# Kernel tuning notes

Hardware: AMD Instinct MI355X
Metric: run time of the kernel (lower is better)

## Reference

```python
import jax, jax.numpy as jnp
import numpy as np

B, N, E = 8, 10000, 160000
F_IN, HID, EMB = 5, 128, 256
A_LAST, S_STEP = 10, 1


def _gcn_layer(x, src, dst, W, b, num_nodes):
    # PyG GCNConv: h = x @ W^T, add self-loops, symmetric norm, scatter-add, + bias
    h = x @ W.T
    loops = jnp.arange(num_nodes, dtype=src.dtype)
    src2 = jnp.concatenate([src, loops])
    dst2 = jnp.concatenate([dst, loops])
    deg = jax.ops.segment_sum(jnp.ones_like(dst2, dtype=h.dtype), dst2, num_segments=num_nodes)
    dinv = jnp.where(deg > 0, jax.lax.rsqrt(deg), 0.0)
    norm = dinv[src2] * dinv[dst2]                     # [E+N]
    msgs = h[src2] * norm[:, None]                     # gather + scale
    out = jax.ops.segment_sum(msgs, dst2, num_segments=num_nodes)
    return out + b


def setup_inputs() -> dict:
    key = jax.random.key(0)
    ks = jax.random.split(key, 14)
    graph_x = jax.random.normal(ks[0], (B, N, F_IN), dtype=jnp.float32)
    graph_edges = jax.random.randint(ks[1], (B, 2, E), 0, N, dtype=jnp.int64)
    position_seq = jax.random.randint(ks[2], (B,), 0, N, dtype=jnp.int64)
    available_moves = jax.random.randint(ks[3], (B, 4), 0, N, dtype=jnp.int64)
    actions = jax.random.normal(ks[4], (B, A_LAST), dtype=jnp.float32)
    steps = jax.random.normal(ks[5], (B, S_STEP), dtype=jnp.float32)

    def glorot(k, shape):
        fan_in = shape[-1]
        return jax.random.normal(k, shape, dtype=jnp.float32) / jnp.sqrt(jnp.float32(fan_in))

    proj_in = HID * 5 + A_LAST + S_STEP
    params = {
        'W1': glorot(ks[6], (HID, F_IN)), 'b1': jnp.zeros((HID,), jnp.float32),
        'W2': glorot(ks[7], (HID, HID)), 'b2': jnp.zeros((HID,), jnp.float32),
        'Wp1': glorot(ks[8], (EMB, proj_in)), 'bp1': jnp.zeros((EMB,), jnp.float32),
        'Wp2': glorot(ks[9], (EMB, EMB)), 'bp2': jnp.zeros((EMB,), jnp.float32),
    }
    return dict(graph_x=graph_x, graph_edges=graph_edges, position_seq=position_seq,
                available_moves=available_moves, actions=actions, steps=steps, **params)


def reference(graph_x, graph_edges, position_seq, available_moves, actions, steps,
              W1, b1, W2, b2, Wp1, bp1, Wp2, bp2):
    b, n, f = graph_x.shape
    num_nodes = b * n
    x = graph_x.reshape(num_nodes, f)
    addition = (jnp.arange(b, dtype=graph_edges.dtype) * n)
    ei = graph_edges + addition[:, None, None]          # [B,2,E]
    ei = jnp.swapaxes(ei, 0, 1).reshape(2, -1)          # [2, B*E]
    src, dst = ei[0], ei[1]
    position = position_seq + addition
    all_positions = jnp.concatenate(
        [available_moves + addition[:, None], position[:, None]], axis=1)  # [B,5]

    x = jax.nn.relu(_gcn_layer(x, src, dst, W1, b1, num_nodes))
    x = jax.nn.relu(_gcn_layer(x, src, dst, W2, b2, num_nodes))

    current_x = x[all_positions].reshape(b, -1)          # [B, 5*HID]
    current_x = jnp.concatenate([current_x, actions, steps], axis=-1)
    h = jax.nn.relu(current_x @ Wp1.T + bp1)
    return h @ Wp2.T + bp2
```

## Files before the change

kernel.cpp:

```cpp
#include <hip/hip_runtime.h>

#define NB 8
#define NN 10000
#define NE 160000
#define NNODES (NB*NN)
#define NEDGE (NB*NE)
#define FIN 5
#define HID 128
#define EMB 256
#define ALAST 10
#define PROJ_IN (HID*5 + ALAST + 1)
#define NPOS 40
#define E0CAP 256
#define TCAP (NPOS + NPOS*E0CAP)
#define E1C 128
#define NBLK ((NNODES+255)/256)

#define C_NT 0
#define C_E0(t) (8 + (t)*16)

__global__ __launch_bounds__(256) void k_init(
        const int* __restrict__ avail, const int* __restrict__ pos,
        int* __restrict__ markT, int* __restrict__ degCnt,
        int* __restrict__ cnts, int* __restrict__ e1cnt,
        int* __restrict__ Tnodes, int* __restrict__ pos2t0,
        int* __restrict__ posNode) {
    __shared__ int pnode[NPOS];
    __shared__ int pslot[NPOS];
    int t = threadIdx.x;
    if (t < 64) {
        int p = t, n = -1;
        if (p < NPOS) {
            int b = p / 5, pi = p - b*5;
            int node = (pi < 4) ? avail[b*4 + pi] : pos[b];
            n = node + b*NN;
        }
        int firstIdx = p;
        for (int q = 0; q < NPOS; ++q) {
            int nq = __shfl(n, q, 64);
            if (p < NPOS && q < p && nq == n && firstIdx == p) firstIdx = q;
        }
        bool isFirst = (p < NPOS) && (firstIdx == p);
        unsigned long long bal = __ballot(isFirst);
        if (p < NPOS) {
            int slot = __popcll(bal & ((1ull << firstIdx) - 1ull));
            pnode[p] = n;
            pslot[p] = slot;
            if (blockIdx.x == 0) {
                pos2t0[p] = slot; posNode[p] = n;
                if (isFirst) Tnodes[slot] = n;
            }
        }
        if (p == 0 && blockIdx.x == 0) cnts[C_NT] = __popcll(bal);
    }
    __syncthreads();
    int i = blockIdx.x*256 + t;
    if (i < NNODES) {
        int mk = -1;
        #pragma unroll
        for (int p = 0; p < NPOS; ++p)
            if (i == pnode[p]) mk = pslot[p];
        markT[i] = mk;
        degCnt[i] = 0;
    }
    if (i >= 1 && i < 1024) cnts[i] = 0;
    for (int j = i; j < TCAP*4; j += NNODES) e1cnt[j] = 0;
}

__global__ __launch_bounds__(256) void k_pass1(const int* __restrict__ edges,
        const int* __restrict__ markT, int* __restrict__ cnts,
        int* __restrict__ e0) {
    int idx = blockIdx.x*256 + threadIdx.x;
    int g = idx / (NE/4), w4 = idx - g*(NE/4);
    const int* base = edges + (size_t)g*2*NE;
    int4 d4 = ((const int4*)(base + NE))[w4];
    int gofs = g*NN;
    int dd[4] = {d4.x, d4.y, d4.z, d4.w};
    #pragma unroll
    for (int c = 0; c < 4; ++c) {
        int t0 = markT[gofs + dd[c]];
        if (t0 >= 0) {
            int s = base[4*w4 + c] + gofs;
            int k = atomicAdd(&cnts[C_E0(t0)], 1);
            if (k < E0CAP) e0[t0*E0CAP + k] = s;
        }
    }
}

__global__ __launch_bounds__(256) void k_dedup(const int* __restrict__ e0,
                        int* __restrict__ cnts, int* __restrict__ markT,
                        int* __restrict__ Tnodes) {
    __shared__ int lc, base;
    int t0 = blockIdx.x;
    if (threadIdx.x == 0) lc = 0;
    __syncthreads();
    int m = cnts[C_E0(t0)]; if (m > E0CAP) m = E0CAP;
    int s = -1, myIdx = -1;
    if ((int)threadIdx.x < m) {
        s = e0[t0*E0CAP + threadIdx.x];
        if (atomicCAS(&markT[s], -1, -2) == -1)
            myIdx = atomicAdd(&lc, 1);
    }
    __syncthreads();
    if (threadIdx.x == 0 && lc > 0) base = atomicAdd(&cnts[C_NT], lc);
    __syncthreads();
    if (myIdx >= 0) {
        int slot = base + myIdx;
        Tnodes[slot] = s;
        markT[s] = slot;
    }
}

__global__ __launch_bounds__(256) void k_pass2(const int* __restrict__ edges,
        int* __restrict__ markT, int* __restrict__ e1cnt, int* __restrict__ e1,
        int* __restrict__ degCnt) {
    int idx = blockIdx.x*256 + threadIdx.x;
    int g = idx / (NE/4), w4 = idx - g*(NE/4);
    const int* base = edges + (size_t)g*2*NE;
    int4 d4 = ((const int4*)(base + NE))[w4];
    int gofs = g*NN;
    int dd[4] = {d4.x, d4.y, d4.z, d4.w};
    #pragma unroll
    for (int c = 0; c < 4; ++c) {
        int d = gofs + dd[c];
        int ts = markT[d];
        if (ts >= 0) {
            int s = base[4*w4 + c] + gofs;
            int k = atomicAdd(&e1cnt[ts*4], 1);
            if (k < E1C) e1[(size_t)ts*E1C + k] = s;
            atomicAdd(&degCnt[d], 1);
            if (markT[s] == -1) markT[s] = -3;
        }
    }
}

__global__ __launch_bounds__(256) void k_pass3(const int* __restrict__ edges,
        const int* __restrict__ markT, int* __restrict__ degCnt) {
    int idx = blockIdx.x*256 + threadIdx.x;
    int g = idx / (NE/4), w4 = idx - g*(NE/4);
    int4 d4 = ((const int4*)(edges + (size_t)g*2*NE + NE))[w4];
    int gofs = g*NN;
    int dd[4] = {d4.x, d4.y, d4.z, d4.w};
    #pragma unroll
    for (int c = 0; c < 4; ++c) {
        int n = gofs + dd[c];
        if (markT[n] == -3) atomicAdd(&degCnt[n], 1);
    }
}

__global__ __launch_bounds__(256) void k_aggT(
        const int* __restrict__ e1cnt, const int* __restrict__ e1,
        const int* __restrict__ degCnt, const int* __restrict__ cnts,
        const float* __restrict__ xg, float* __restrict__ axT) {
    int slot = blockIdx.x*4 + (threadIdx.x >> 6);
    int lane = threadIdx.x & 63;
    int ntv = cnts[C_NT]; if (ntv > TCAP) ntv = TCAP;
    if (slot >= ntv) return;
    int m = e1cnt[slot*4]; if (m > E1C) m = E1C;
    float acc[FIN] = {0.f, 0.f, 0.f, 0.f, 0.f};
    for (int j = lane; j < m; j += 64) {
        int s = e1[(size_t)slot*E1C + j];
        float dv = rsqrtf(1.0f + (float)degCnt[s]);
        const float* xr = xg + (size_t)s*FIN;
        #pragma unroll
        for (int f = 0; f < FIN; ++f) acc[f] += xr[f]*dv;
    }
    #pragma unroll
    for (int f = 0; f < FIN; ++f) {
        #pragma unroll
        for (int d = 32; d; d >>= 1) acc[f] += __shfl_down(acc[f], d, 64);
    }
    if (lane == 0) {
        #pragma unroll
        for (int f = 0; f < FIN; ++f) axT[(size_t)slot*FIN + f] = acc[f];
    }
}

#define KC 32
__global__ __launch_bounds__(256) void k_h12T(
        const float* __restrict__ axT, const int* __restrict__ Tnodes,
        const int* __restrict__ degCnt, const int* __restrict__ cnts,
        const float* __restrict__ xg,
        const float* __restrict__ W1, const float* __restrict__ b1,
        const float* __restrict__ W2, float* __restrict__ hsT) {
    __shared__ float axs[FIN][128];
    __shared__ float w1s[FIN][128];
    __shared__ float b1s[128];
    __shared__ float dvs[128];
    __shared__ float xs[KC*128];
    __shared__ float wt[KC*64];
    int ntv = cnts[C_NT]; if (ntv > TCAP) ntv = TCAP;
    int jb  = blockIdx.x & 1;
    int m0g = (blockIdx.x >> 1) * 128;
    if (m0g >= ntv) return;
    int tid = threadIdx.x;
    if (tid < 128) {
        b1s[tid] = b1[tid];
        #pragma unroll
        for (int f = 0; f < FIN; ++f) w1s[f][tid] = W1[tid*FIN + f];
    } else {
        int r2 = tid - 128;
        int row = m0g + r2;
        int ok = row < ntv;
        int node = ok ? Tnodes[row] : 0;
        float dvv = ok ? rsqrtf(1.0f + (float)degCnt[node]) : 0.0f;
        dvs[r2] = dvv;
        #pragma unroll
        for (int f = 0; f < FIN; ++f)
            axs[f][r2] = ok ? (axT[(size_t)row*FIN + f]
                               + xg[(size_t)node*FIN + f]*dvv) : 0.0f;
    }
    int tx = tid & 15, ty = tid >> 4;
    int m0 = ty*8;
    int j0 = tx*4;
    int r  = tid >> 1;
    int kq = (tid & 1) * 16;
    int rw  = tid >> 2;
    int kqw = (tid & 3) * 8;
    float a[8][4];
    #pragma unroll
    for (int i = 0; i < 8; ++i)
        #pragma unroll
        for (int j = 0; j < 4; ++j) a[i][j] = 0.f;
    __syncthreads();
    float axr[FIN];
    float dvr = dvs[r];
    #pragma unroll
    for (int f = 0; f < FIN; ++f) axr[f] = axs[f][r] * dvr;

    for (int kh = 0; kh < 128; kh += KC) {
        float4 wv0 = *(const float4*)&W2[(size_t)(jb*64 + rw)*128 + kh + kqw];
        float4 wv1 = *(const float4*)&W2[(size_t)(jb*64 + rw)*128 + kh + kqw + 4];
        float hv[16];
        #pragma unroll
        for (int kk = 0; kk < 16; ++kk) {
            int k1 = kh + kq + kk;
            float sv = b1s[k1];
            #pragma unroll
            for (int f = 0; f < FIN; ++f) sv += axr[f]*w1s[f][k1];
            hv[kk] = fmaxf(sv, 0.0f);
        }
        __syncthreads();
        #pragma unroll
        for (int kk = 0; kk < 16; ++kk) xs[(kq+kk)*128 + r] = hv[kk];
        wt[(kqw+0)*64 + rw] = wv0.x;
        wt[(kqw+1)*64 + rw] = wv0.y;
        wt[(kqw+2)*64 + rw] = wv0.z;
        wt[(kqw+3)*64 + rw] = wv0.w;
        wt[(kqw+4)*64 + rw] = wv1.x;
        wt[(kqw+5)*64 + rw] = wv1.y;
        wt[(kqw+6)*64 + rw] = wv1.z;
        wt[(kqw+7)*64 + rw] = wv1.w;
        __syncthreads();
        for (int k = 0; k < KC; ++k) {
            float4 xa = *(const float4*)&xs[k*128 + m0];
            float4 xb = *(const float4*)&xs[k*128 + m0 + 4];
            float4 wa = *(const float4*)&wt[k*64 + j0];
            float xr[8] = {xa.x,xa.y,xa.z,xa.w,xb.x,xb.y,xb.z,xb.w};
            #pragma unroll
            for (int i = 0; i < 8; ++i) {
                a[i][0] += xr[i]*wa.x;
                a[i][1] += xr[i]*wa.y;
                a[i][2] += xr[i]*wa.z;
                a[i][3] += xr[i]*wa.w;
            }
        }
    }
    #pragma unroll
    for (int i = 0; i < 8; ++i) {
        int row = m0g + m0 + i;
        if (row < ntv) {
            float dv = dvs[m0 + i];
            float4 v0 = make_float4(a[i][0]*dv, a[i][1]*dv, a[i][2]*dv, a[i][3]*dv);
            *(float4*)&hsT[(size_t)row*HID + jb*64 + j0] = v0;
        }
    }
}

__global__ __launch_bounds__(256) void k_mlp1(
        const int* __restrict__ pos2t0, const int* __restrict__ posNode,
        const int* __restrict__ e1cnt, const int* __restrict__ e1,
        const int* __restrict__ markT, const float* __restrict__ hsT,
        const int* __restrict__ degCnt, const float* __restrict__ b2,
        const float* __restrict__ actions, const float* __restrict__ steps,
        const float* __restrict__ Wp1, const float* __restrict__ bp1,
        float* __restrict__ hm) {
    int b  = blockIdx.x >> 4;
    int jg = blockIdx.x & 15;
    int t  = threadIdx.x;
    __shared__ float c[PROJ_IN];
    __shared__ int slots[5*E1C];
    __shared__ int cm[5], t0s[5];
    __shared__ float dvP[5];
    if (t < 5) {
        int t0 = pos2t0[b*5 + t];
        t0s[t] = t0;
        int m = e1cnt[t0*4]; if (m > E1C) m = E1C;
        cm[t] = m;
        dvP[t] = rsqrtf(1.0f + (float)degCnt[posNode[b*5 + t]]);
    }
    __syncthreads();
    for (int i = t; i < 5*E1C; i += 256) {
        int p5 = i >> 7, j = i & (E1C-1);
        if (j < cm[p5]) slots[i] = markT[e1[(size_t)t0s[p5]*E1C + j]];
    }
    __syncthreads();
    for (int i = t; i < 5*HID; i += 256) {
        int p5 = i >> 7, f = i & 127;
        float acc = hsT[(size_t)t0s[p5]*HID + f];
        int m = cm[p5];
        const int* sp = &slots[p5*E1C];
        for (int j = 0; j < m; ++j) {
            int ts = sp[j];
            if (ts >= 0) acc += hsT[(size_t)ts*HID + f];
        }
        c[i] = fmaxf(acc*dvP[p5] + b2[f], 0.0f);
    }
    if (t < ALAST) c[5*HID + t] = actions[b*ALAST + t];
    if (t == ALAST) c[5*HID + ALAST] = steps[b];
    __syncthreads();
    int o = t >> 4, sub = t & 15;
    int j = jg*16 + o;
    const float* wr = Wp1 + (size_t)j*PROJ_IN;
    float s = 0.f;
    for (int k = sub; k < PROJ_IN; k += 16) s += c[k]*wr[k];
    #pragma unroll
    for (int d = 8; d; d >>= 1) s += __shfl_down(s, d, 16);
    if (sub == 0) hm[b*EMB + j] = fmaxf(s + bp1[j], 0.f);
}

__global__ __launch_bounds__(256) void k_mlp2(
        const float* __restrict__ hm, const float* __restrict__ Wp2,
        const float* __restrict__ bp2, float* __restrict__ out) {
    int b  = blockIdx.x >> 4;
    int jg = blockIdx.x & 15;
    int t  = threadIdx.x;
    __shared__ float c[EMB];
    if (t < EMB) c[t] = hm[b*EMB + t];
    __syncthreads();
    int o = t >> 4, sub = t & 15;
    int j = jg*16 + o;
    const float* wr = Wp2 + (size_t)j*EMB;
    float s = 0.f;
    for (int k = sub; k < EMB; k += 16) s += c[k]*wr[k];
    #pragma unroll
    for (int d = 8; d; d >>= 1) s += __shfl_down(s, d, 16);
    if (sub == 0) out[b*EMB + j] = s + bp2[j];
}

extern "C" void kernel_launch(void* const* d_in, const int* in_sizes, int n_in,
                              void* d_out, int out_size, void* d_ws, size_t ws_size,
                              hipStream_t stream) {
    const float* graph_x = (const float*)d_in[0];
    const int*   edges   = (const int*)d_in[1];
    const int*   pos     = (const int*)d_in[2];
    const int*   avail   = (const int*)d_in[3];
    const float* actions = (const float*)d_in[4];
    const float* steps   = (const float*)d_in[5];
    const float* W1  = (const float*)d_in[6];
    const float* b1  = (const float*)d_in[7];
    const float* W2  = (const float*)d_in[8];
    const float* b2  = (const float*)d_in[9];
    const float* Wp1 = (const float*)d_in[10];
    const float* bp1 = (const float*)d_in[11];
    const float* Wp2 = (const float*)d_in[12];
    const float* bp2 = (const float*)d_in[13];
    float* out = (float*)d_out;

    char* ws = (char*)d_ws;
    size_t off = 0;
    #define ALLOC(ptrname, type, nelem) \
        type* ptrname = (type*)(ws + off); off = (off + (size_t)(nelem)*sizeof(type) + 255) & ~(size_t)255;
    ALLOC(markT,   int,   NNODES)
    ALLOC(degCnt,  int,   NNODES)
    ALLOC(cnts,    int,   1024)
    ALLOC(e1cnt,   int,   TCAP*4)
    ALLOC(Tnodes,  int,   TCAP)
    ALLOC(pos2t0,  int,   NPOS)
    ALLOC(posNode, int,   NPOS)
    ALLOC(e0,      int,   NPOS*E0CAP)
    ALLOC(e1,      int,   (size_t)TCAP*E1C)
    ALLOC(axT,     float, (size_t)(TCAP+128)*FIN)
    ALLOC(hsT,     float, (size_t)TCAP*HID)
    ALLOC(hm,      float, (size_t)NB*EMB)
    #undef ALLOC

    k_init<<<NBLK, 256, 0, stream>>>(avail, pos, markT, degCnt, cnts, e1cnt,
                                     Tnodes, pos2t0, posNode);
    k_pass1<<<NEDGE/4/256, 256, 0, stream>>>(edges, markT, cnts, e0);
    k_dedup<<<NPOS, 256, 0, stream>>>(e0, cnts, markT, Tnodes);
    k_pass2<<<NEDGE/4/256, 256, 0, stream>>>(edges, markT, e1cnt, e1, degCnt);
    k_pass3<<<NEDGE/4/256, 256, 0, stream>>>(edges, markT, degCnt);
    k_aggT<<<(TCAP+3)/4, 256, 0, stream>>>(e1cnt, e1, degCnt, cnts, graph_x, axT);
    k_h12T<<<2*((TCAP+127)/128), 256, 0, stream>>>(axT, Tnodes, degCnt, cnts,
                                                   graph_x, W1, b1, W2, hsT);
    k_mlp1<<<NB*16, 256, 0, stream>>>(pos2t0, posNode, e1cnt, e1, markT, hsT,
                                      degCnt, b2, actions, steps, Wp1, bp1, hm);
    k_mlp2<<<NB*16, 256, 0, stream>>>(hm, Wp2, bp2, out);
}
```

Measured before the change: 166.1 us.

## Fuse all pipeline stages into one cooperative persistent kernel with grid syncs

Merges the nine separate kernel launches into a single cooperative kernel that walks the same stages with grid-stride loops separated by grid-wide barriers, with a shared-memory union sized for the largest stage. It targets launch overhead and inter-kernel gaps in a pipeline of short dependent kernels. The trade-off is grid-sync cost and a grid capped by occupancy (up to 1280 blocks), which may lower parallelism for the edge passes. If the cooperative launch fails, it falls back to the old multi-kernel path.

```diff
diff --git a/kernel.cpp b/kernel.cpp
--- a/kernel.cpp
+++ b/kernel.cpp
@@ -1,4 +1,6 @@
 #include <hip/hip_runtime.h>
+#include <hip/hip_cooperative_groups.h>
+namespace cg = cooperative_groups;
 
 #define NB 8
 #define NN 10000
@@ -15,9 +17,347 @@
 #define TCAP (NPOS + NPOS*E0CAP)
 #define E1C 128
 #define NBLK ((NNODES+255)/256)
+#define KC 32
 
 #define C_NT 0
 #define C_E0(t) (8 + (t)*16)
+
+struct SmemH12 {
+    float axs[FIN][128];
+    float w1s[FIN][128];
+    float b1s[128];
+    float dvs[128];
+    float xs[KC*128];
+    float wt[KC*64];
+};
+struct SmemMlp1 {
+    float c[PROJ_IN];
+    int slots[5*E1C];
+    int cm[5], t0s[5];
+    float dvP[5];
+};
+struct SmemInit { int pnode[NPOS]; int pslot[NPOS]; };
+struct SmemDD   { int lc; int base; };
+union SmemAll {
+    SmemH12  h12;
+    SmemMlp1 m1;
+    SmemInit init;
+    SmemDD   dd;
+    float    c2[EMB];
+};
+
+__global__ __launch_bounds__(256, 4) void k_all(
+        const float* __restrict__ xg, const int* __restrict__ edges,
+        const int* __restrict__ pos, const int* __restrict__ avail,
+        const float* __restrict__ actions, const float* __restrict__ steps,
+        const float* __restrict__ W1, const float* __restrict__ b1,
+        const float* __restrict__ W2, const float* __restrict__ b2,
+        const float* __restrict__ Wp1, const float* __restrict__ bp1,
+        const float* __restrict__ Wp2, const float* __restrict__ bp2,
+        float* __restrict__ out,
+        int* __restrict__ markT, int* __restrict__ degCnt,
+        int* __restrict__ cnts, int* __restrict__ e1cnt,
+        int* __restrict__ Tnodes, int* __restrict__ pos2t0,
+        int* __restrict__ posNode, int* __restrict__ e0,
+        int* __restrict__ e1, float* __restrict__ axT,
+        float* __restrict__ hsT, float* __restrict__ hm)
+{
+    cg::grid_group gg = cg::this_grid();
+    __shared__ SmemAll sm;
+    const int tid  = threadIdx.x;
+    const int bid  = blockIdx.x;
+    const int nbk  = gridDim.x;
+    const int gtid = bid*256 + tid;
+    const int nthr = nbk*256;
+
+    if (tid < 64) {
+        int p = tid, n = -1;
+        if (p < NPOS) {
+            int b = p / 5, pi = p - b*5;
+            int node = (pi < 4) ? avail[b*4 + pi] : pos[b];
+            n = node + b*NN;
+        }
+        int firstIdx = p;
+        for (int q = 0; q < NPOS; ++q) {
+            int nq = __shfl(n, q, 64);
+            if (p < NPOS && q < p && nq == n && firstIdx == p) firstIdx = q;
+        }
+        bool isFirst = (p < NPOS) && (firstIdx == p);
+        unsigned long long bal = __ballot(isFirst);
+        if (p < NPOS) {
+            int slot = __popcll(bal & ((1ull << firstIdx) - 1ull));
+            sm.init.pnode[p] = n;
+            sm.init.pslot[p] = slot;
+            if (bid == 0) {
+                pos2t0[p] = slot; posNode[p] = n;
+                if (isFirst) Tnodes[slot] = n;
+            }
+        }
+        if (p == 0 && bid == 0) cnts[C_NT] = __popcll(bal);
+    }
+    __syncthreads();
+    for (int i = gtid; i < NNODES; i += nthr) {
+        int mk = -1;
+        #pragma unroll
+        for (int p = 0; p < NPOS; ++p)
+            if (i == sm.init.pnode[p]) mk = sm.init.pslot[p];
+        markT[i] = mk;
+        degCnt[i] = 0;
+    }
+    for (int i = gtid; i < 1024; i += nthr) if (i != C_NT) cnts[i] = 0;
+    for (int j = gtid; j < TCAP*4; j += nthr) e1cnt[j] = 0;
+    gg.sync();
+
+    for (int q = gtid; q < NEDGE/4; q += nthr) {
+        int g = q / (NE/4), w4 = q - g*(NE/4);
+        const int* base = edges + (size_t)g*2*NE;
+        int4 d4 = ((const int4*)(base + NE))[w4];
+        int gofs = g*NN;
+        int dd4[4] = {d4.x, d4.y, d4.z, d4.w};
+        #pragma unroll
+        for (int c = 0; c < 4; ++c) {
+            int t0 = markT[gofs + dd4[c]];
+            if (t0 >= 0) {
+                int s = base[4*w4 + c] + gofs;
+                int k = atomicAdd(&cnts[C_E0(t0)], 1);
+                if (k < E0CAP) e0[t0*E0CAP + k] = s;
+            }
+        }
+    }
+    gg.sync();
+
+    if (bid < NPOS) {
+        if (tid == 0) sm.dd.lc = 0;
+        __syncthreads();
+        int m = cnts[C_E0(bid)]; if (m > E0CAP) m = E0CAP;
+        int s = -1, myIdx = -1;
+        if (tid < m) {
+            s = e0[bid*E0CAP + tid];
+            if (atomicCAS(&markT[s], -1, -2) == -1)
+                myIdx = atomicAdd(&sm.dd.lc, 1);
+        }
+        __syncthreads();
+        if (tid == 0 && sm.dd.lc > 0) sm.dd.base = atomicAdd(&cnts[C_NT], sm.dd.lc);
+        __syncthreads();
+        if (myIdx >= 0) {
+            int slot = sm.dd.base + myIdx;
+            Tnodes[slot] = s;
+            markT[s] = slot;
+        }
+    }
+    gg.sync();
+
+    for (int q = gtid; q < NEDGE/4; q += nthr) {
+        int g = q / (NE/4), w4 = q - g*(NE/4);
+        const int* base = edges + (size_t)g*2*NE;
+        int4 d4 = ((const int4*)(base + NE))[w4];
+        int gofs = g*NN;
+        int dd4[4] = {d4.x, d4.y, d4.z, d4.w};
+        #pragma unroll
+        for (int c = 0; c < 4; ++c) {
+            int d = gofs + dd4[c];
+            int ts = markT[d];
+            if (ts >= 0) {
+                int s = base[4*w4 + c] + gofs;
+                int k = atomicAdd(&e1cnt[ts*4], 1);
+                if (k < E1C) e1[(size_t)ts*E1C + k] = s;
+                atomicAdd(&degCnt[d], 1);
+                if (markT[s] == -1) markT[s] = -3;
+            }
+        }
+    }
+    gg.sync();
+
+    for (int q = gtid; q < NEDGE/4; q += nthr) {
+        int g = q / (NE/4), w4 = q - g*(NE/4);
+        int4 d4 = ((const int4*)(edges + (size_t)g*2*NE + NE))[w4];
+        int gofs = g*NN;
+        int dd4[4] = {d4.x, d4.y, d4.z, d4.w};
+        #pragma unroll
+        for (int c = 0; c < 4; ++c) {
+            int n = gofs + dd4[c];
+            if (markT[n] == -3) atomicAdd(&degCnt[n], 1);
+        }
+    }
+    gg.sync();
+
+    int ntv = cnts[C_NT]; if (ntv > TCAP) ntv = TCAP;
+    {
+        int lane = tid & 63;
+        for (int slot = bid*4 + (tid >> 6); slot < ntv; slot += nbk*4) {
+            int m = e1cnt[slot*4]; if (m > E1C) m = E1C;
+            float acc[FIN] = {0.f, 0.f, 0.f, 0.f, 0.f};
+            for (int j = lane; j < m; j += 64) {
+                int s = e1[(size_t)slot*E1C + j];
+                float dv = rsqrtf(1.0f + (float)degCnt[s]);
+                const float* xr = xg + (size_t)s*FIN;
+                #pragma unroll
+                for (int f = 0; f < FIN; ++f) acc[f] += xr[f]*dv;
+            }
+            #pragma unroll
+            for (int f = 0; f < FIN; ++f) {
+                #pragma unroll
+                for (int d = 32; d; d >>= 1) acc[f] += __shfl_down(acc[f], d, 64);
+            }
+            if (lane == 0) {
+                #pragma unroll
+                for (int f = 0; f < FIN; ++f) axT[(size_t)slot*FIN + f] = acc[f];
+            }
+        }
+    }
+    gg.sync();
+
+    {
+        int nblk6 = 2*((ntv + 127)/128);
+        int tx = tid & 15, ty = tid >> 4;
+        int m0 = ty*8, j0 = tx*4;
+        int r  = tid >> 1, kq = (tid & 1)*16;
+        int rw = tid >> 2, kqw = (tid & 3)*8;
+        for (int b6 = bid; b6 < nblk6; b6 += nbk) {
+            int jb  = b6 & 1;
+            int m0g = (b6 >> 1)*128;
+            if (tid < 128) {
+                sm.h12.b1s[tid] = b1[tid];
+                #pragma unroll
+                for (int f = 0; f < FIN; ++f) sm.h12.w1s[f][tid] = W1[tid*FIN + f];
+            } else {
+                int r2 = tid - 128;
+                int row = m0g + r2;
+                int ok = row < ntv;
+                int node = ok ? Tnodes[row] : 0;
+                float dvv = ok ? rsqrtf(1.0f + (float)degCnt[node]) : 0.0f;
+                sm.h12.dvs[r2] = dvv;
+                #pragma unroll
+                for (int f = 0; f < FIN; ++f)
+                    sm.h12.axs[f][r2] = ok ? (axT[(size_t)row*FIN + f]
+                                              + xg[(size_t)node*FIN + f]*dvv) : 0.0f;
+            }
+            float a[8][4];
+            #pragma unroll
+            for (int i = 0; i < 8; ++i)
+                #pragma unroll
+                for (int j = 0; j < 4; ++j) a[i][j] = 0.f;
+            __syncthreads();
+            float axr[FIN];
+            float dvr = sm.h12.dvs[r];
+            #pragma unroll
+            for (int f = 0; f < FIN; ++f) axr[f] = sm.h12.axs[f][r] * dvr;
+
+            for (int kh = 0; kh < 128; kh += KC) {
+                float4 wv0 = *(const float4*)&W2[(size_t)(jb*64 + rw)*128 + kh + kqw];
+                float4 wv1 = *(const float4*)&W2[(size_t)(jb*64 + rw)*128 + kh + kqw + 4];
+                float hv[16];
+                #pragma unroll
+                for (int kk = 0; kk < 16; ++kk) {
+                    int k1 = kh + kq + kk;
+                    float sv = sm.h12.b1s[k1];
+                    #pragma unroll
+                    for (int f = 0; f < FIN; ++f) sv += axr[f]*sm.h12.w1s[f][k1];
+                    hv[kk] = fmaxf(sv, 0.0f);
+                }
+                __syncthreads();
+                #pragma unroll
+                for (int kk = 0; kk < 16; ++kk) sm.h12.xs[(kq+kk)*128 + r] = hv[kk];
+                sm.h12.wt[(kqw+0)*64 + rw] = wv0.x;
+                sm.h12.wt[(kqw+1)*64 + rw] = wv0.y;
+                sm.h12.wt[(kqw+2)*64 + rw] = wv0.z;
+                sm.h12.wt[(kqw+3)*64 + rw] = wv0.w;
+                sm.h12.wt[(kqw+4)*64 + rw] = wv1.x;
+                sm.h12.wt[(kqw+5)*64 + rw] = wv1.y;
+                sm.h12.wt[(kqw+6)*64 + rw] = wv1.z;
+                sm.h12.wt[(kqw+7)*64 + rw] = wv1.w;
+                __syncthreads();
+                for (int k = 0; k < KC; ++k) {
+                    float4 xa = *(const float4*)&sm.h12.xs[k*128 + m0];
+                    float4 xb = *(const float4*)&sm.h12.xs[k*128 + m0 + 4];
+                    float4 wa = *(const float4*)&sm.h12.wt[k*64 + j0];
+                    float xr[8] = {xa.x,xa.y,xa.z,xa.w,xb.x,xb.y,xb.z,xb.w};
+                    #pragma unroll
+                    for (int i = 0; i < 8; ++i) {
+                        a[i][0] += xr[i]*wa.x;
+                        a[i][1] += xr[i]*wa.y;
+                        a[i][2] += xr[i]*wa.z;
+                        a[i][3] += xr[i]*wa.w;
+                    }
+                }
+            }
+            #pragma unroll
+            for (int i = 0; i < 8; ++i) {
+                int row = m0g + m0 + i;
+                if (row < ntv) {
+                    float dv = sm.h12.dvs[m0 + i];
+                    float4 v0 = make_float4(a[i][0]*dv, a[i][1]*dv, a[i][2]*dv, a[i][3]*dv);
+                    *(float4*)&hsT[(size_t)row*HID + jb*64 + j0] = v0;
+                }
+            }
+            __syncthreads();
+        }
+    }
+    gg.sync();
+
+    for (int b7 = bid; b7 < NB*16; b7 += nbk) {
+        int b  = b7 >> 4;
+        int jg = b7 & 15;
+        if (tid < 5) {
+            int t0 = pos2t0[b*5 + tid];
+            sm.m1.t0s[tid] = t0;
+            int m = e1cnt[t0*4]; if (m > E1C) m = E1C;
+            sm.m1.cm[tid] = m;
+            sm.m1.dvP[tid] = rsqrtf(1.0f + (float)degCnt[posNode[b*5 + tid]]);
+        }
+        __syncthreads();
+        for (int i = tid; i < 5*E1C; i += 256) {
+            int p5 = i >> 7, j = i & (E1C-1);
+            if (j < sm.m1.cm[p5]) sm.m1.slots[i] = markT[e1[(size_t)sm.m1.t0s[p5]*E1C + j]];
+        }
+        __syncthreads();
+        for (int i = tid; i < 5*HID; i += 256) {
+            int p5 = i >> 7, f = i & 127;
+            float acc = hsT[(size_t)sm.m1.t0s[p5]*HID + f];
+            int m = sm.m1.cm[p5];
+            const int* sp = &sm.m1.slots[p5*E1C];
+            for (int j = 0; j < m; ++j) {
+                int ts = sp[j];
+                if (ts >= 0) acc += hsT[(size_t)ts*HID + f];
+            }
+            sm.m1.c[i] = fmaxf(acc*sm.m1.dvP[p5] + b2[f], 0.0f);
+        }
+        if (tid < ALAST) sm.m1.c[5*HID + tid] = actions[b*ALAST + tid];
+        if (tid == ALAST) sm.m1.c[5*HID + ALAST] = steps[b];
+        __syncthreads();
+        {
+            int o = tid >> 4, sub = tid & 15;
+            int j = jg*16 + o;
+            const float* wr = Wp1 + (size_t)j*PROJ_IN;
+            float s = 0.f;
+            for (int k = sub; k < PROJ_IN; k += 16) s += sm.m1.c[k]*wr[k];
+            #pragma unroll
+            for (int d = 8; d; d >>= 1) s += __shfl_down(s, d, 16);
+            if (sub == 0) hm[b*EMB + j] = fmaxf(s + bp1[j], 0.f);
+        }
+        __syncthreads();
+    }
+    gg.sync();
+
+    for (int b8 = bid; b8 < NB*16; b8 += nbk) {
+        int b  = b8 >> 4;
+        int jg = b8 & 15;
+        if (tid < EMB) sm.c2[tid] = hm[b*EMB + tid];
+        __syncthreads();
+        {
+            int o = tid >> 4, sub = tid & 15;
+            int j = jg*16 + o;
+            const float* wr = Wp2 + (size_t)j*EMB;
+            float s = 0.f;
+            for (int k = sub; k < EMB; k += 16) s += sm.c2[k]*wr[k];
+            #pragma unroll
+            for (int d = 8; d; d >>= 1) s += __shfl_down(s, d, 16);
+            if (sub == 0) out[b*EMB + j] = s + bp2[j];
+        }
+        __syncthreads();
+    }
+}
+
 
 __global__ __launch_bounds__(256) void k_init(
         const int* __restrict__ avail, const int* __restrict__ pos,
@@ -176,7 +516,6 @@
     }
 }
 
-#define KC 32
 __global__ __launch_bounds__(256) void k_h12T(
         const float* __restrict__ axT, const int* __restrict__ Tnodes,
         const int* __restrict__ degCnt, const int* __restrict__ cnts,
@@ -385,6 +724,25 @@
     ALLOC(hm,      float, (size_t)NB*EMB)
     #undef ALLOC
 
+    static int s_grid = 0;
+    if (s_grid == 0) {
+        int nbm = 0;
+        if (hipOccupancyMaxActiveBlocksPerMultiprocessor(&nbm, k_all, 256, 0) != hipSuccess
+            || nbm < 1) nbm = 4;
+        long g = (long)nbm * 256;
+        if (g > 1280) g = 1280;
+        if (g < 64)   g = 64;
+        s_grid = (int)g;
+    }
+    void* params[] = { &graph_x, &edges, &pos, &avail, &actions, &steps,
+                       &W1, &b1, &W2, &b2, &Wp1, &bp1, &Wp2, &bp2, &out,
+                       &markT, &degCnt, &cnts, &e1cnt, &Tnodes, &pos2t0,
+                       &posNode, &e0, &e1, &axT, &hsT, &hm };
+    hipError_t err = hipLaunchCooperativeKernel((void*)k_all, dim3(s_grid), dim3(256),
+                                                params, 0, stream);
+    if (err == hipSuccess) return;
+
+    (void)hipGetLastError();
     k_init<<<NBLK, 256, 0, stream>>>(avail, pos, markT, degCnt, cnts, e1cnt,
                                      Tnodes, pos2t0, posNode);
     k_pass1<<<NEDGE/4/256, 256, 0, stream>>>(edges, markT, cnts, e0);
```

New measurement: 610.2 us. +267.4%, slower.
